# Kernel tuning notes

Hardware: AMD Instinct MI355X
Metric: run time of the kernel (lower is better)

The kernel has to match this reference:

```python
import jax, jax.numpy as jnp
import numpy as np

N1 = 50000; N2 = 50000; E1 = 800000; E2 = 800000; A = 10000
D_IN = 128; NHID = 128; D_OUT = 128; RATIO = 0.5
N_SUP = int(N1 * RATIO)  # 25000 super nodes
K_HOPS = 10  # GCN(in, nhid, k=10)
NEG_INF = jnp.float32(-1e30)


def _edge_norm(src, dst, w, n):
    # symmetric degree normalization of edge weights
    deg = jax.ops.segment_sum(w, dst, num_segments=n) + 1.0
    return w * jax.lax.rsqrt(deg[src] * deg[dst])


def _prop(h, src, dst, norm, n):
    # one round of weighted message passing: h'[v] = sum_e norm_e * h[src_e]
    return jax.ops.segment_sum(norm[:, None] * h[src], dst, num_segments=n)


def _gcn_k(x, src, dst, norm, n, W, b):
    h = x @ W + b
    for _ in range(K_HOPS):
        h = _prop(h, src, dst, norm, n)
    return h


def setup_inputs() -> dict:
    key = jax.random.key(0)
    ks = jax.random.split(key, 24)
    s = 0.05
    return {
        "x": jax.random.normal(ks[0], (N1, D_IN), jnp.float32),
        "edge_index": jax.random.randint(ks[1], (2, E1), 0, N1, jnp.int32),
        "edge_weight": jax.random.uniform(ks[2], (E1,), jnp.float32),
        "y": jax.random.normal(ks[3], (N2, D_IN), jnp.float32),
        "edge_index_y": jax.random.randint(ks[4], (2, E2), 0, N2, jnp.int32),
        "edge_weight_y": jax.random.uniform(ks[5], (E2,), jnp.float32),
        "anchor_links": jax.random.randint(ks[6], (2, A), 0, N1, jnp.int32),
        "temperature": 1,
        "W_gcn": jax.random.normal(ks[7], (D_IN, NHID), jnp.float32) * s,
        "b_gcn": jnp.zeros((NHID,), jnp.float32),
        "p_score": jax.random.normal(ks[8], (NHID,), jnp.float32) * s,
        "W_conv1": jax.random.normal(ks[9], (NHID, NHID), jnp.float32) * s,
        "b_conv1": jnp.zeros((NHID,), jnp.float32),
        "W_mlp1": jax.random.normal(ks[10], (NHID, NHID), jnp.float32) * s,
        "b_mlp1": jnp.zeros((NHID,), jnp.float32),
        "W_l1": jax.random.normal(ks[11], (NHID, NHID), jnp.float32) * s,
        "W_l2": jax.random.normal(ks[12], (NHID, NHID), jnp.float32) * s,
        "W_mlp2": jax.random.normal(ks[13], (NHID, D_OUT), jnp.float32) * s,
        "b_mlp2": jnp.zeros((D_OUT,), jnp.float32),
    }


def reference(x, edge_index, edge_weight, y, edge_index_y, edge_weight_y,
              anchor_links, temperature, W_gcn, b_gcn, p_score, W_conv1,
              b_conv1, W_mlp1, b_mlp1, W_l1, W_l2, W_mlp2, b_mlp2):
    T = jnp.float32(temperature)
    src, dst = edge_index[0], edge_index[1]
    norm1 = _edge_norm(src, dst, edge_weight, N1)

    # ---- down_convs[0]: 10-hop GCN on graph 1 ----
    out_x = _gcn_k(x, src, dst, norm1, N1, W_gcn, b_gcn)  # xs[0]
    xr = jax.nn.relu(out_x)

    # ---- TransPool: score -> top-k super nodes -> attention assignment ----
    s = xr @ p_score                             # [N1]
    _, perm = jax.lax.top_k(s, N_SUP)            # original ids of super nodes
    sup_id = jnp.full((N1,), -1, jnp.int32).at[perm].set(
        jnp.arange(N_SUP, dtype=jnp.int32))
    self_ids = jnp.arange(N1, dtype=src.dtype)
    cand_node = jnp.concatenate([src, self_ids])  # node being assigned
    cand_sup = jnp.concatenate([dst, self_ids])   # candidate super node
    valid = sup_id[cand_sup] >= 0
    att = jnp.sum(xr[cand_node] * xr[cand_sup], axis=-1)
    att = att / (jnp.sqrt(jnp.float32(NHID)) * T)
    att = jnp.where(valid, att, NEG_INF)
    m = jax.ops.segment_max(att, cand_node, num_segments=N1)
    e = jnp.exp(att - m[cand_node])
    esum = jax.ops.segment_sum(e, cand_node, num_segments=N1)
    w_soft = e / esum[cand_node]                 # per-node softmax over candidates
    is_best = valid & (att >= m[cand_node])
    cluster = jnp.full((N1,), -1, jnp.int32).at[cand_node].max(
        jnp.where(is_best, sup_id[cand_sup], -1))
    has = cluster >= 0
    cluster = jnp.maximum(cluster, 0)
    match = is_best & (sup_id[cand_sup] == cluster[cand_node])
    a = jnp.zeros((N1,), jnp.float32).at[cand_node].max(
        jnp.where(match, w_soft, 0.0))
    a = jnp.where(has, a, 0.0)                   # assign_weight (P1 values)

    # coarsen: x' = P x ; A' = P A P^T via cluster relabeling
    x_pool = jax.ops.segment_sum(a[:, None] * xr, cluster, num_segments=N_SUP)
    csrc, cdst = cluster[src], cluster[dst]
    cw = edge_weight * a[src] * a[dst]

    # ---- down_convs[1]: GCNConv on coarse graph (with self loop) ----
    norm_c = _edge_norm(csrc, cdst, cw, N_SUP)
    h2 = x_pool @ W_conv1 + b_conv1
    h2 = _prop(h2, csrc, cdst, norm_c, N_SUP) + h2
    sup1 = jax.nn.relu(h2)                       # xs[1]

    # ---- MLP1 ----
    sup2 = jax.nn.relu(sup1 @ W_mlp1 + b_mlp1)

    # ---- Q = P1 @ L (sparse-sparse matmul) ----
    a1, a2 = anchor_links[0], anchor_links[1]
    anchor_w = jnp.ones((A,), jnp.float32)
    q_sup = cluster[a1]
    q_col = a2
    q_w = a[a1] * anchor_w

    # ---- graph 2: shared down_convs[0] ----
    srcy, dsty = edge_index_y[0], edge_index_y[1]
    normy = _edge_norm(srcy, dsty, edge_weight_y, N2)
    out_y = _gcn_k(y, srcy, dsty, normy, N2, W_gcn, b_gcn)

    # ---- LastLayer: Q^T (sup2 W_l1) + L^T (out_x W_l2) scattered into graph2 ----
    t1 = sup2 @ W_l1
    out_y = out_y + jax.ops.segment_sum(q_w[:, None] * t1[q_sup], q_col,
                                        num_segments=N2)
    t2 = out_x @ W_l2
    out_y = out_y + jax.ops.segment_sum(anchor_w[:, None] * t2[a1], a2,
                                        num_segments=N2)

    recon_y = out_y @ W_mlp2 + b_mlp2
    return (out_x, sup1, out_y, sup2, a, recon_y)
```

## Files before the change

kernel.cpp:

```cpp
#include <hip/hip_runtime.h>
#include <hip/hip_bf16.h>
#include <math.h>

#define N1 50000
#define N2 50000
#define E1C 800000
#define E2C 800000
#define AC 10000
#define F 128
#define NSUP 25000
#define KHOPS 10
#define NEGINF -1e30f
#define NBINS 65536
#define NBINS22 (1 << 22)

static inline int cdiv(int a, int b) { return (a + b - 1) / b; }

__device__ __forceinline__ float bf2f(unsigned short u) {
  return __uint_as_float(((unsigned)u) << 16);
}
__device__ __forceinline__ unsigned short f2bf(float f) {
  unsigned x = __float_as_uint(f);
  return (unsigned short)((x + 0x7FFFu + ((x >> 16) & 1u)) >> 16);
}

__global__ void k_count(const int* __restrict__ key, int* __restrict__ cnt, int n) {
  int e = blockIdx.x * blockDim.x + threadIdx.x;
  if (e < n) atomicAdd(&cnt[key[e]], 1);
}

__global__ void k_scan(const int* __restrict__ cnt, int* __restrict__ rowptr, int n) {
  const int T = 1024;
  int t = threadIdx.x;
  int vpt = (n + T - 1) / T;
  int lo = t * vpt, hi = lo + vpt;
  if (hi > n) hi = n;
  int sum = 0;
  for (int i = lo; i < hi; ++i) sum += cnt[i];
  int lane = t & 63, wid = t >> 6;
  int v = sum;
#pragma unroll
  for (int o = 1; o < 64; o <<= 1) {
    int u = __shfl_up(v, o, 64);
    if (lane >= o) v += u;
  }
  __shared__ int wsum[16];
  if (lane == 63) wsum[wid] = v;
  __syncthreads();
  if (t < 16) {
    int w = wsum[t];
#pragma unroll
    for (int o = 1; o < 16; o <<= 1) {
      int u = __shfl_up(w, o, 64);
      if (t >= o) w += u;
    }
    wsum[t] = w;
  }
  __syncthreads();
  int base = (wid ? wsum[wid - 1] : 0) + (v - sum);
  if (t == 0) rowptr[0] = 0;
  int run = base;
  for (int i = lo; i < hi; ++i) { run += cnt[i]; rowptr[i + 1] = run; }
}

__global__ void k_fill(const int* __restrict__ key, const int* __restrict__ payload,
                       const float* __restrict__ val, const int* __restrict__ rowptr,
                       int* __restrict__ cnt, int* __restrict__ col, float* __restrict__ v,
                       int n) {
  int e = blockIdx.x * blockDim.x + threadIdx.x;
  if (e < n) {
    int k = key[e];
    int p = atomicAdd(&cnt[k], 1);
    int s = rowptr[k] + p;
    col[s] = payload[e];
    if (val) v[s] = val[e];
  }
}

__global__ void k_fill_iota(const int* __restrict__ key, const int* __restrict__ rowptr,
                            int* __restrict__ cnt, int* __restrict__ col, int n) {
  int e = blockIdx.x * blockDim.x + threadIdx.x;
  if (e < n) {
    int k = key[e];
    int p = atomicAdd(&cnt[k], 1);
    col[rowptr[k] + p] = e;
  }
}

__global__ void k_count_coarse(const int* __restrict__ dst, const int* __restrict__ cluster,
                               int* __restrict__ cnt, int n) {
  int e = blockIdx.x * blockDim.x + threadIdx.x;
  if (e < n) atomicAdd(&cnt[cluster[dst[e]]], 1);
}

__global__ void k_fill_coarse(const int* __restrict__ src, const int* __restrict__ dst,
                              const int* __restrict__ cluster, const float* __restrict__ w,
                              const float* __restrict__ a, const int* __restrict__ rowptr,
                              int* __restrict__ cnt, int* __restrict__ col,
                              float* __restrict__ v, int n) {
  int e = blockIdx.x * blockDim.x + threadIdx.x;
  if (e < n) {
    int sd = dst[e];
    int k = cluster[sd];
    int p = atomicAdd(&cnt[k], 1);
    int s = rowptr[k] + p;
    int ss = src[e];
    col[s] = cluster[ss];
    v[s] = w[e] * a[ss] * a[sd];
  }
}

__global__ void k_rowsum(const int* __restrict__ rowptr, const float* __restrict__ v,
                         float* __restrict__ deg, int n) {
  int row = blockIdx.x * 8 + (threadIdx.x >> 5);
  if (row >= n) return;
  int q = threadIdx.x & 31;
  int s0 = rowptr[row], s1 = rowptr[row + 1];
  float s = 0.f;
  for (int k = s0 + q; k < s1; k += 32) s += v[k];
#pragma unroll
  for (int o = 16; o; o >>= 1) s += __shfl_xor(s, o, 64);
  if (q == 0) deg[row] = s;
}

__global__ void k_csrnorm(const int* __restrict__ rowptr, const int* __restrict__ col,
                          float* __restrict__ v, const float* __restrict__ deg, int n) {
  int row = blockIdx.x * 8 + (threadIdx.x >> 5);
  if (row >= n) return;
  int q = threadIdx.x & 31;
  int s0 = rowptr[row], s1 = rowptr[row + 1];
  float di = deg[row] + 1.f;
  for (int s = s0 + q; s < s1; s += 32) {
    float dc = deg[col[s]] + 1.f;
    v[s] = v[s] / sqrtf(dc * di);
  }
}

__global__ void k_prop(const float4* __restrict__ hin, float4* __restrict__ hout,
                       float4* __restrict__ relu_out, const int* __restrict__ rowptr,
                       const int* __restrict__ col, const float* __restrict__ val, int n) {
  int node = blockIdx.x * 8 + (threadIdx.x >> 5);
  if (node >= n) return;
  int q = threadIdx.x & 31;
  int grp = threadIdx.x & 32;
  int s0 = rowptr[node], s1 = rowptr[node + 1];
  float4 acc = make_float4(0.f, 0.f, 0.f, 0.f);
  for (int s = s0; s < s1; s += 32) {
    int es = s + q;
    int ok = es < s1;
    int sc = ok ? es : (s1 - 1);
    int cme = col[sc];
    float vme = ok ? val[sc] : 0.f;
    int nb = s1 - s; if (nb > 32) nb = 32;
    for (int j = 0; j < nb; j += 8) {
      int c8[8]; float v8[8];
#pragma unroll
      for (int t = 0; t < 8; ++t) {
        c8[t] = __shfl(cme, grp + j + t, 64);
        v8[t] = __shfl(vme, grp + j + t, 64);
      }
      float4 h[8];
#pragma unroll
      for (int t = 0; t < 8; ++t) h[t] = hin[(size_t)c8[t] * 32 + q];
#pragma unroll
      for (int t = 0; t < 8; ++t) {
        acc.x = fmaf(v8[t], h[t].x, acc.x);
        acc.y = fmaf(v8[t], h[t].y, acc.y);
        acc.z = fmaf(v8[t], h[t].z, acc.z);
        acc.w = fmaf(v8[t], h[t].w, acc.w);
      }
    }
  }
  hout[(size_t)node * 32 + q] = acc;
  if (relu_out) {
    float4 r;
    r.x = fmaxf(acc.x, 0.f); r.y = fmaxf(acc.y, 0.f);
    r.z = fmaxf(acc.z, 0.f); r.w = fmaxf(acc.w, 0.f);
    relu_out[(size_t)node * 32 + q] = r;
  }
}

__global__ void k_prop_dual(const float4* __restrict__ hin1, float4* __restrict__ hout1,
                            float4* __restrict__ xr_out,
                            const int* __restrict__ rp1, const int* __restrict__ col1,
                            const float* __restrict__ val1,
                            const ushort4* __restrict__ hin2, ushort4* __restrict__ hout2,
                            float4* __restrict__ fout2,
                            const int* __restrict__ rp2, const int* __restrict__ col2,
                            const float* __restrict__ val2, int n) {
  int node = (blockIdx.x >> 1) * 8 + (threadIdx.x >> 5);
  if (node >= n) return;
  int q = threadIdx.x & 31;
  int grp = threadIdx.x & 32;
  if ((blockIdx.x & 1) == 0) {
    int s0 = rp1[node], s1 = rp1[node + 1];
    float4 acc = make_float4(0.f, 0.f, 0.f, 0.f);
    for (int s = s0; s < s1; s += 32) {
      int es = s + q;
      int ok = es < s1;
      int sc = ok ? es : (s1 - 1);
      int cme = col1[sc];
      float vme = ok ? val1[sc] : 0.f;
      int nb = s1 - s; if (nb > 32) nb = 32;
      for (int j = 0; j < nb; j += 8) {
        int c8[8]; float v8[8];
#pragma unroll
        for (int t = 0; t < 8; ++t) {
          c8[t] = __shfl(cme, grp + j + t, 64);
          v8[t] = __shfl(vme, grp + j + t, 64);
        }
        float4 h[8];
#pragma unroll
        for (int t = 0; t < 8; ++t) h[t] = hin1[(size_t)c8[t] * 32 + q];
#pragma unroll
        for (int t = 0; t < 8; ++t) {
          acc.x = fmaf(v8[t], h[t].x, acc.x);
          acc.y = fmaf(v8[t], h[t].y, acc.y);
          acc.z = fmaf(v8[t], h[t].z, acc.z);
          acc.w = fmaf(v8[t], h[t].w, acc.w);
        }
      }
    }
    hout1[(size_t)node * 32 + q] = acc;
    if (xr_out) {
      float4 r;
      r.x = fmaxf(acc.x, 0.f); r.y = fmaxf(acc.y, 0.f);
      r.z = fmaxf(acc.z, 0.f); r.w = fmaxf(acc.w, 0.f);
      xr_out[(size_t)node * 32 + q] = r;
    }
  } else {
    int s0 = rp2[node], s1 = rp2[node + 1];
    float4 acc = make_float4(0.f, 0.f, 0.f, 0.f);
    for (int s = s0; s < s1; s += 32) {
      int es = s + q;
      int ok = es < s1;
      int sc = ok ? es : (s1 - 1);
      int cme = col2[sc];
      float vme = ok ? val2[sc] : 0.f;
      int nb = s1 - s; if (nb > 32) nb = 32;
      for (int j = 0; j < nb; j += 8) {
        int c8[8]; float v8[8];
#pragma unroll
        for (int t = 0; t < 8; ++t) {
          c8[t] = __shfl(cme, grp + j + t, 64);
          v8[t] = __shfl(vme, grp + j + t, 64);
        }
        ushort4 h[8];
#pragma unroll
        for (int t = 0; t < 8; ++t) h[t] = hin2[(size_t)c8[t] * 32 + q];
#pragma unroll
        for (int t = 0; t < 8; ++t) {
          acc.x = fmaf(v8[t], bf2f(h[t].x), acc.x);
          acc.y = fmaf(v8[t], bf2f(h[t].y), acc.y);
          acc.z = fmaf(v8[t], bf2f(h[t].z), acc.z);
          acc.w = fmaf(v8[t], bf2f(h[t].w), acc.w);
        }
      }
    }
    if (fout2) {
      fout2[(size_t)node * 32 + q] = acc;
    } else {
      ushort4 o;
      o.x = f2bf(acc.x); o.y = f2bf(acc.y); o.z = f2bf(acc.z); o.w = f2bf(acc.w);
      hout2[(size_t)node * 32 + q] = o;
    }
  }
}

__global__ void k_transpose(const float* __restrict__ W, float* __restrict__ WT) {
  int i = blockIdx.x * blockDim.x + threadIdx.x;
  if (i < F * F) { int k = i >> 7, c = i & 127; WT[c * F + k] = W[i]; }
}

__global__ void k_mm128(const float* __restrict__ X, const float* __restrict__ WT,
                        const float* __restrict__ bias, float* __restrict__ out,
                        int M, int relu) {
  __shared__ float4 xs[16][32];
  int tid = threadIdx.x;
  int c = tid & 127;
  int half = tid >> 7;
  int row0 = blockIdx.x * 16;
  for (int t = tid; t < 512; t += 256) {
    int r = t >> 5, k4 = t & 31;
    int gr = row0 + r;
    float4 v = make_float4(0.f, 0.f, 0.f, 0.f);
    if (gr < M) v = ((const float4*)X)[(size_t)gr * 32 + k4];
    xs[r][k4] = v;
  }
  __syncthreads();
  float acc[8];
#pragma unroll
  for (int r = 0; r < 8; ++r) acc[r] = 0.f;
  const float4* wrow = (const float4*)WT + (size_t)c * 32;
  for (int k4 = 0; k4 < 32; ++k4) {
    float4 w = wrow[k4];
#pragma unroll
    for (int r = 0; r < 8; ++r) {
      float4 xv = xs[half * 8 + r][k4];
      acc[r] = fmaf(xv.x, w.x, acc[r]);
      acc[r] = fmaf(xv.y, w.y, acc[r]);
      acc[r] = fmaf(xv.z, w.z, acc[r]);
      acc[r] = fmaf(xv.w, w.w, acc[r]);
    }
  }
  float bb = bias ? bias[c] : 0.f;
#pragma unroll
  for (int r = 0; r < 8; ++r) {
    int gr = row0 + half * 8 + r;
    if (gr < M) {
      float v = acc[r] + bb;
      if (relu) v = fmaxf(v, 0.f);
      out[(size_t)gr * F + c] = v;
    }
  }
}

__global__ void k_mm128_bf16(const float* __restrict__ X, const float* __restrict__ WT,
                             const float* __restrict__ bias, unsigned short* __restrict__ out,
                             int M) {
  __shared__ float4 xs[16][32];
  int tid = threadIdx.x;
  int c = tid & 127;
  int half = tid >> 7;
  int row0 = blockIdx.x * 16;
  for (int t = tid; t < 512; t += 256) {
    int r = t >> 5, k4 = t & 31;
    int gr = row0 + r;
    float4 v = make_float4(0.f, 0.f, 0.f, 0.f);
    if (gr < M) v = ((const float4*)X)[(size_t)gr * 32 + k4];
    xs[r][k4] = v;
  }
  __syncthreads();
  float acc[8];
#pragma unroll
  for (int r = 0; r < 8; ++r) acc[r] = 0.f;
  const float4* wrow = (const float4*)WT + (size_t)c * 32;
  for (int k4 = 0; k4 < 32; ++k4) {
    float4 w = wrow[k4];
#pragma unroll
    for (int r = 0; r < 8; ++r) {
      float4 xv = xs[half * 8 + r][k4];
      acc[r] = fmaf(xv.x, w.x, acc[r]);
      acc[r] = fmaf(xv.y, w.y, acc[r]);
      acc[r] = fmaf(xv.z, w.z, acc[r]);
      acc[r] = fmaf(xv.w, w.w, acc[r]);
    }
  }
  float bb = bias ? bias[c] : 0.f;
#pragma unroll
  for (int r = 0; r < 8; ++r) {
    int gr = row0 + half * 8 + r;
    if (gr < M) out[(size_t)gr * F + c] = f2bf(acc[r] + bb);
  }
}

__global__ void k_addrelu(const float* __restrict__ a, const float* __restrict__ b,
                          float* __restrict__ out, int n) {
  int i = blockIdx.x * blockDim.x + threadIdx.x;
  if (i < n) out[i] = fmaxf(a[i] + b[i], 0.f);
}

__global__ void k_score(const float* __restrict__ xr, const float* __restrict__ p,
                        float* __restrict__ s, int n) {
  int wid = (blockIdx.x * blockDim.x + threadIdx.x) >> 6;
  int lane = threadIdx.x & 63;
  if (wid >= n) return;
  const float* row = xr + (size_t)wid * F;
  float d = row[lane] * p[lane] + row[lane + 64] * p[lane + 64];
#pragma unroll
  for (int o = 32; o; o >>= 1) d += __shfl_xor(d, o, 64);
  if (lane == 0) s[wid] = d;
}

__device__ __forceinline__ unsigned sortkey(float f) {
  if (f == 0.f) f = 0.f;
  unsigned u = __float_as_uint(f);
  return (u & 0x80000000u) ? ~u : (u | 0x80000000u);
}

__global__ void k_key(const float* __restrict__ s, unsigned* __restrict__ key, int n) {
  int i = blockIdx.x * blockDim.x + threadIdx.x;
  if (i < n) key[i] = sortkey(s[i]);
}

__global__ void k_count_bins22(const unsigned* __restrict__ key, int* __restrict__ cnt, int n) {
  int i = blockIdx.x * blockDim.x + threadIdx.x;
  if (i < n) atomicAdd(&cnt[key[i] >> 10], 1);
}

__global__ void k_hist_blocksum(const int* __restrict__ cnt, int* __restrict__ partial) {
  int t = threadIdx.x;
  int base = blockIdx.x * 1024 + t * 4;
  int s = cnt[base] + cnt[base + 1] + cnt[base + 2] + cnt[base + 3];
#pragma unroll
  for (int o = 32; o; o >>= 1) s += __shfl_down(s, o, 64);
  __shared__ int ws[4];
  int lane = t & 63, w = t >> 6;
  if (lane == 0) ws[w] = s;
  __syncthreads();
  if (t == 0) partial[blockIdx.x] = ws[0] + ws[1] + ws[2] + ws[3];
}

__global__ void k_hist_apply(const int* __restrict__ cnt, const int* __restrict__ partialptr,
                             int* __restrict__ binptr) {
  int t = threadIdx.x;
  int base = blockIdx.x * 1024 + t * 4;
  int c0 = cnt[base], c1 = cnt[base + 1], c2 = cnt[base + 2], c3 = cnt[base + 3];
  int s = c0 + c1 + c2 + c3;
  int lane = t & 63, w = t >> 6;
  int v = s;
#pragma unroll
  for (int o = 1; o < 64; o <<= 1) {
    int u = __shfl_up(v, o, 64);
    if (lane >= o) v += u;
  }
  __shared__ int ws[4];
  if (lane == 63) ws[w] = v;
  __syncthreads();
  int wb = 0;
  for (int i = 0; i < w; ++i) wb += ws[i];
  int run = partialptr[blockIdx.x] + wb + (v - s);
  binptr[base + 1] = run + c0;
  binptr[base + 2] = run + c0 + c1;
  binptr[base + 3] = run + c0 + c1 + c2;
  binptr[base + 4] = run + s;
  if (blockIdx.x == 0 && t == 0) binptr[0] = 0;
}

__global__ void k_fill_bins22(const unsigned* __restrict__ key, const int* __restrict__ binptr,
                              int* __restrict__ cnt, int* __restrict__ bidx,
                              unsigned* __restrict__ bkey, int n) {
  int i = blockIdx.x * blockDim.x + threadIdx.x;
  if (i < n) {
    unsigned k = key[i];
    int b = k >> 10;
    int p = atomicAdd(&cnt[b], 1);
    int s = binptr[b] + p;
    bidx[s] = i;
    bkey[s] = k;
  }
}

__global__ void k_rank22(const unsigned* __restrict__ key, const int* __restrict__ binptr,
                         const int* __restrict__ bidx, const unsigned* __restrict__ bkey,
                         int* __restrict__ supid, int n) {
  int i = blockIdx.x * blockDim.x + threadIdx.x;
  if (i >= n) return;
  unsigned ki = key[i];
  int b = ki >> 10;
  int cnt = n - binptr[b + 1];
  int s1 = binptr[b + 1];
  for (int s = binptr[b]; s < s1; ++s) {
    unsigned kj = bkey[s];
    cnt += (kj > ki) || (kj == ki && bidx[s] < i);
  }
  supid[i] = (cnt < NSUP) ? cnt : -1;
}

__device__ __forceinline__ float read_T(const void* p) {
  int ib = *(const int*)p;
  float fb = __int_as_float(ib);
  if (ib >= 1 && ib < (1 << 20)) return (float)ib;
  if (fb > 1e-6f && fb < 1e6f) return fb;
  return 1.0f;
}

__global__ void k_att_a(const float* __restrict__ xr, const int* __restrict__ rowptr,
                        const int* __restrict__ col, const int* __restrict__ supid,
                        const void* __restrict__ tptr, float* __restrict__ att,
                        float* __restrict__ attself, float* __restrict__ mout, int n) {
  int wid = (blockIdx.x * blockDim.x + threadIdx.x) >> 6;
  int lane = threadIdx.x & 63;
  if (wid >= n) return;
  float inv = 1.0f / (sqrtf(128.0f) * read_T(tptr));
  const float* xn = xr + (size_t)wid * F;
  float x0 = xn[lane], x1 = xn[lane + 64];
  float d = x0 * x0 + x1 * x1;
#pragma unroll
  for (int o = 32; o; o >>= 1) d += __shfl_xor(d, o, 64);
  float av = (supid[wid] >= 0) ? d * inv : NEGINF;
  float m = av;
  if (lane == 0) attself[wid] = av;
  int s0 = rowptr[wid], s1 = rowptr[wid + 1];
  for (int s = s0; s < s1; s += 4) {
    int c[4]; bool ok[4];
#pragma unroll
    for (int j = 0; j < 4; ++j) {
      int ss = s + j;
      ok[j] = ss < s1;
      c[j] = col[ok[j] ? ss : (s1 - 1)];
    }
    float dd[4];
#pragma unroll
    for (int j = 0; j < 4; ++j) {
      const float* xc = xr + (size_t)c[j] * F;
      dd[j] = x0 * xc[lane] + x1 * xc[lane + 64];
    }
#pragma unroll
    for (int j = 0; j < 4; ++j) {
#pragma unroll
      for (int o = 32; o; o >>= 1) dd[j] += __shfl_xor(dd[j], o, 64);
    }
#pragma unroll
    for (int j = 0; j < 4; ++j) {
      if (ok[j]) {
        float a2 = (supid[c[j]] >= 0) ? dd[j] * inv : NEGINF;
        if (lane == 0) att[s + j] = a2;
        m = fmaxf(m, a2);
      }
    }
  }
  if (lane == 0) mout[wid] = m;
}

__global__ void k_att_b(const int* __restrict__ rowptr, const int* __restrict__ col,
                        const int* __restrict__ supid, const float* __restrict__ att,
                        const float* __restrict__ attself, const float* __restrict__ mv,
                        int* __restrict__ cluster, float* __restrict__ aout, int n) {
  int i = blockIdx.x * 8 + (threadIdx.x >> 5);
  if (i >= n) return;
  int q = threadIdx.x & 31;
  float m = mv[i];
  float as = attself[i];
  float esum = 0.f;
  int best = -1;
  if (q == 0) {
    esum = expf(as - m);
    if (as >= m) best = supid[i];
  }
  int s0 = rowptr[i], s1 = rowptr[i + 1];
  for (int s = s0 + q; s < s1; s += 32) {
    float av = att[s];
    esum += expf(av - m);
    if (av >= m) {
      int sid = supid[col[s]];
      if (sid > best) best = sid;
    }
  }
#pragma unroll
  for (int o = 16; o; o >>= 1) {
    esum += __shfl_xor(esum, o, 64);
    int ob = __shfl_xor(best, o, 64);
    if (ob > best) best = ob;
  }
  if (q == 0) {
    int has = best >= 0;
    cluster[i] = has ? best : 0;
    aout[i] = has ? 1.0f / esum : 0.0f;
  }
}

__global__ void k_xpool_pull(const float4* __restrict__ xr, const float* __restrict__ a,
                             const int* __restrict__ rowptrM, const int* __restrict__ memb,
                             float4* __restrict__ xpool, int n) {
  int c = blockIdx.x * 8 + (threadIdx.x >> 5);
  if (c >= n) return;
  int q = threadIdx.x & 31;
  int s0 = rowptrM[c], s1 = rowptrM[c + 1];
  float4 acc = make_float4(0.f, 0.f, 0.f, 0.f);
  for (int s = s0; s < s1; ++s) {
    int m = memb[s];
    float av = a[m];
    float4 h = xr[(size_t)m * 32 + q];
    acc.x = fmaf(av, h.x, acc.x);
    acc.y = fmaf(av, h.y, acc.y);
    acc.z = fmaf(av, h.z, acc.z);
    acc.w = fmaf(av, h.w, acc.w);
  }
  xpool[(size_t)c * 32 + q] = acc;
}

__global__ void k_scatter_q(const int* __restrict__ a1, const int* __restrict__ a2,
                            const int* __restrict__ cluster, const float* __restrict__ aarr,
                            const float* __restrict__ t1, float* __restrict__ outy, int nA) {
  int idx = blockIdx.x * blockDim.x + threadIdx.x;
  if (idx >= nA * F) return;
  int k = idx >> 7, f = idx & 127;
  int n1 = a1[k];
  float qw = aarr[n1];
  if (qw != 0.f)
    atomicAdd(&outy[(size_t)a2[k] * F + f], qw * t1[(size_t)cluster[n1] * F + f]);
}

__global__ void k_scatter_t2(const int* __restrict__ a1, const int* __restrict__ a2,
                             const float* __restrict__ t2, float* __restrict__ outy, int nA) {
  int idx = blockIdx.x * blockDim.x + threadIdx.x;
  if (idx >= nA * F) return;
  int k = idx >> 7, f = idx & 127;
  atomicAdd(&outy[(size_t)a2[k] * F + f], t2[(size_t)a1[k] * F + f]);
}

extern "C" void kernel_launch(void* const* d_in, const int* in_sizes, int n_in,
                              void* d_out, int out_size, void* d_ws, size_t ws_size,
                              hipStream_t stream) {
  (void)in_sizes; (void)n_in; (void)out_size; (void)ws_size;
  const float* x   = (const float*)d_in[0];
  const int*   ei  = (const int*)d_in[1];
  const float* w1  = (const float*)d_in[2];
  const float* y   = (const float*)d_in[3];
  const int*   eiy = (const int*)d_in[4];
  const float* wy  = (const float*)d_in[5];
  const int*   anc = (const int*)d_in[6];
  const void*  tmp = d_in[7];
  const float* W_gcn = (const float*)d_in[8];
  const float* b_gcn = (const float*)d_in[9];
  const float* p_sc  = (const float*)d_in[10];
  const float* W_c1  = (const float*)d_in[11];
  const float* b_c1  = (const float*)d_in[12];
  const float* W_m1  = (const float*)d_in[13];
  const float* b_m1  = (const float*)d_in[14];
  const float* W_l1  = (const float*)d_in[15];
  const float* W_l2  = (const float*)d_in[16];
  const float* W_m2  = (const float*)d_in[17];
  const float* b_m2  = (const float*)d_in[18];

  float* out   = (float*)d_out;
  float* out_x = out;
  float* sup1  = out_x + (size_t)N1 * F;
  float* out_y = sup1 + (size_t)NSUP * F;
  float* sup2  = out_y + (size_t)N2 * F;
  float* a_out = sup2 + (size_t)NSUP * F;
  float* recon = a_out + N1;

  char* wsb = (char*)d_ws;
  size_t off = 0;
  auto alloc = [&](size_t bytes) -> void* {
    void* p = wsb + off;
    off = (off + bytes + 255) & ~(size_t)255;
    return p;
  };
  float*    f_csr1v   = (float*)alloc((size_t)E1C * 4);
  int*      i_csr1c   = (int*)alloc((size_t)E1C * 4);
  int*      i_rowptr1 = (int*)alloc((size_t)(N1 + 1) * 4);
  int*      i_rowptr2 = (int*)alloc((size_t)(N2 + 1) * 4);
  float*    f_deg     = (float*)alloc((size_t)N1 * 4);
  int*      i_cnt     = (int*)alloc((size_t)(NBINS + 1) * 4);
  float*    f_ha      = (float*)alloc((size_t)N1 * F * 4);
  float*    f_hb      = (float*)alloc((size_t)N1 * F * 4);
  float*    f_xr      = (float*)alloc((size_t)N1 * F * 4);
  float*    f_s       = (float*)alloc((size_t)N1 * 4);
  unsigned* u_key     = (unsigned*)alloc((size_t)N1 * 4);
  int*      i_partial = (int*)alloc((size_t)4096 * 4);
  int*      i_partptr = (int*)alloc((size_t)4097 * 4);
  int*      i_bidx    = (int*)alloc((size_t)N1 * 4);
  unsigned* u_bkey    = (unsigned*)alloc((size_t)N1 * 4);
  int*      i_supid   = (int*)alloc((size_t)N1 * 4);
  int*      i_rowptrS = (int*)alloc((size_t)(N1 + 1) * 4);
  int*      i_csrSc   = (int*)alloc((size_t)E1C * 4);
  float*    f_att     = (float*)alloc((size_t)E1C * 4);
  float*    f_attself = (float*)alloc((size_t)N1 * 4);
  float*    f_m       = (float*)alloc((size_t)N1 * 4);
  int*      i_cluster = (int*)alloc((size_t)N1 * 4);
  float*    f_xpool   = (float*)alloc((size_t)NSUP * F * 4);
  float*    f_degc    = (float*)alloc((size_t)NSUP * 4);
  int*      i_rowptrC = (int*)alloc((size_t)(NSUP + 1) * 4);
  int*      i_csrCc   = (int*)alloc((size_t)E1C * 4);
  float*    f_csrCv   = (float*)alloc((size_t)E1C * 4);
  int*      i_rowptrM = (int*)alloc((size_t)(NSUP + 1) * 4);
  int*      i_memb    = (int*)alloc((size_t)N1 * 4);
  float*    f_h2      = (float*)alloc((size_t)NSUP * F * 4);
  float*    f_h2p     = (float*)alloc((size_t)NSUP * F * 4);
  float*    f_wt      = (float*)alloc((size_t)6 * F * F * 4);

  int* i_cnt22    = (int*)f_ha;
  int* i_binptr22 = (int*)f_hb;
  int*   i_csr2c  = i_csrCc;
  float* f_csr2v  = f_csrCv;
  unsigned short* h16a = (unsigned short*)f_xpool;
  unsigned short* h16b = (unsigned short*)f_h2;

  const int* src1 = ei,  * dst1 = ei + E1C;
  const int* srcy = eiy, * dsty = eiy + E2C;
  const int* a1 = anc, * a2 = anc + AC;

  const float* Ws[6] = { W_gcn, W_c1, W_m1, W_l1, W_l2, W_m2 };
  for (int i = 0; i < 6; ++i)
    k_transpose<<<cdiv(F * F, 256), 256, 0, stream>>>(Ws[i], f_wt + (size_t)i * F * F);
  float* wt_gcn = f_wt, *wt_c1 = f_wt + 16384, *wt_m1 = f_wt + 2 * 16384,
       * wt_l1 = f_wt + 3 * 16384, *wt_l2 = f_wt + 4 * 16384, *wt_m2 = f_wt + 5 * 16384;

  int gE = cdiv(E1C, 256);
  int gN = cdiv(N1, 256);
  int gN8 = cdiv(N1, 8);
  int gC8 = cdiv(NSUP, 8);
  int gD = 2 * cdiv(N1, 8);

  hipMemsetAsync(i_cnt, 0, (size_t)(NBINS + 1) * 4, stream);
  k_count<<<gE, 256, 0, stream>>>(dst1, i_cnt, E1C);
  k_scan<<<1, 1024, 0, stream>>>(i_cnt, i_rowptr1, N1);
  hipMemsetAsync(i_cnt, 0, (size_t)(NBINS + 1) * 4, stream);
  k_fill<<<gE, 256, 0, stream>>>(dst1, src1, w1, i_rowptr1, i_cnt, i_csr1c, f_csr1v, E1C);
  k_rowsum<<<gN8, 256, 0, stream>>>(i_rowptr1, f_csr1v, f_deg, N1);
  k_csrnorm<<<gN8, 256, 0, stream>>>(i_rowptr1, i_csr1c, f_csr1v, f_deg, N1);

  hipMemsetAsync(i_cnt, 0, (size_t)(NBINS + 1) * 4, stream);
  k_count<<<gE, 256, 0, stream>>>(dsty, i_cnt, E2C);
  k_scan<<<1, 1024, 0, stream>>>(i_cnt, i_rowptr2, N2);
  hipMemsetAsync(i_cnt, 0, (size_t)(NBINS + 1) * 4, stream);
  k_fill<<<gE, 256, 0, stream>>>(dsty, srcy, wy, i_rowptr2, i_cnt, i_csr2c, f_csr2v, E2C);
  k_rowsum<<<gN8, 256, 0, stream>>>(i_rowptr2, f_csr2v, f_deg, N2);
  k_csrnorm<<<gN8, 256, 0, stream>>>(i_rowptr2, i_csr2c, f_csr2v, f_deg, N2);

  k_mm128<<<cdiv(N1, 16), 256, 0, stream>>>(x, wt_gcn, b_gcn, f_ha, N1, 0);
  k_mm128_bf16<<<cdiv(N2, 16), 256, 0, stream>>>(y, wt_gcn, b_gcn, h16a, N2);

  {
    const float* cur1 = f_ha;
    const unsigned short* cur2 = h16a;
    for (int i = 0; i < KHOPS; ++i) {
      int last = (i == KHOPS - 1);
      float* dst1b = last ? out_x : ((i & 1) ? f_ha : f_hb);
      unsigned short* dst2b = (i & 1) ? h16a : h16b;
      k_prop_dual<<<gD, 256, 0, stream>>>(
          (const float4*)cur1, (float4*)dst1b, last ? (float4*)f_xr : nullptr,
          i_rowptr1, i_csr1c, f_csr1v,
          (const ushort4*)cur2, (ushort4*)dst2b, last ? (float4*)out_y : nullptr,
          i_rowptr2, i_csr2c, f_csr2v, N1);
      cur1 = dst1b; cur2 = dst2b;
    }
  }

  k_score<<<cdiv(N1, 4), 256, 0, stream>>>(f_xr, p_sc, f_s, N1);
  k_key<<<gN, 256, 0, stream>>>(f_s, u_key, N1);
  hipMemsetAsync(i_cnt22, 0, (size_t)NBINS22 * 4, stream);
  k_count_bins22<<<gN, 256, 0, stream>>>(u_key, i_cnt22, N1);
  k_hist_blocksum<<<NBINS22 / 1024, 256, 0, stream>>>(i_cnt22, i_partial);
  k_scan<<<1, 1024, 0, stream>>>(i_partial, i_partptr, 4096);
  k_hist_apply<<<NBINS22 / 1024, 256, 0, stream>>>(i_cnt22, i_partptr, i_binptr22);
  hipMemsetAsync(i_cnt22, 0, (size_t)NBINS22 * 4, stream);
  k_fill_bins22<<<gN, 256, 0, stream>>>(u_key, i_binptr22, i_cnt22, i_bidx, u_bkey, N1);
  k_rank22<<<gN, 256, 0, stream>>>(u_key, i_binptr22, i_bidx, u_bkey, i_supid, N1);

  hipMemsetAsync(i_cnt, 0, (size_t)(NBINS + 1) * 4, stream);
  k_count<<<gE, 256, 0, stream>>>(src1, i_cnt, E1C);
  k_scan<<<1, 1024, 0, stream>>>(i_cnt, i_rowptrS, N1);
  hipMemsetAsync(i_cnt, 0, (size_t)(NBINS + 1) * 4, stream);
  k_fill<<<gE, 256, 0, stream>>>(src1, dst1, (const float*)nullptr, i_rowptrS, i_cnt, i_csrSc,
                                 (float*)nullptr, E1C);

  k_att_a<<<cdiv(N1, 4), 256, 0, stream>>>(f_xr, i_rowptrS, i_csrSc, i_supid, tmp,
                                           f_att, f_attself, f_m, N1);
  k_att_b<<<gN8, 256, 0, stream>>>(i_rowptrS, i_csrSc, i_supid, f_att, f_attself,
                                   f_m, i_cluster, a_out, N1);

  hipMemsetAsync(i_cnt, 0, (size_t)(NBINS + 1) * 4, stream);
  k_count<<<gN, 256, 0, stream>>>(i_cluster, i_cnt, N1);
  k_scan<<<1, 1024, 0, stream>>>(i_cnt, i_rowptrM, NSUP);
  hipMemsetAsync(i_cnt, 0, (size_t)(NBINS + 1) * 4, stream);
  k_fill_iota<<<gN, 256, 0, stream>>>(i_cluster, i_rowptrM, i_cnt, i_memb, N1);
  k_xpool_pull<<<gC8, 256, 0, stream>>>((const float4*)f_xr, a_out, i_rowptrM,
                                        i_memb, (float4*)f_xpool, NSUP);

  hipMemsetAsync(i_cnt, 0, (size_t)(NBINS + 1) * 4, stream);
  k_count_coarse<<<gE, 256, 0, stream>>>(dst1, i_cluster, i_cnt, E1C);
  k_scan<<<1, 1024, 0, stream>>>(i_cnt, i_rowptrC, NSUP);
  hipMemsetAsync(i_cnt, 0, (size_t)(NBINS + 1) * 4, stream);
  k_fill_coarse<<<gE, 256, 0, stream>>>(src1, dst1, i_cluster, w1, a_out, i_rowptrC, i_cnt,
                                        i_csrCc, f_csrCv, E1C);
  k_rowsum<<<gC8, 256, 0, stream>>>(i_rowptrC, f_csrCv, f_degc, NSUP);
  k_csrnorm<<<gC8, 256, 0, stream>>>(i_rowptrC, i_csrCc, f_csrCv, f_degc, NSUP);

  k_mm128<<<cdiv(NSUP, 16), 256, 0, stream>>>(f_xpool, wt_c1, b_c1, f_h2, NSUP, 0);
  k_prop<<<gC8, 256, 0, stream>>>((const float4*)f_h2, (float4*)f_h2p, nullptr,
                                  i_rowptrC, i_csrCc, f_csrCv, NSUP);
  k_addrelu<<<cdiv(NSUP * F, 256), 256, 0, stream>>>(f_h2p, f_h2, sup1, NSUP * F);
  k_mm128<<<cdiv(NSUP, 16), 256, 0, stream>>>(sup1, wt_m1, b_m1, sup2, NSUP, 1);

  float* f_t1 = f_h2p;
  float* f_t2 = f_xr;
  k_mm128<<<cdiv(NSUP, 16), 256, 0, stream>>>(sup2, wt_l1, (const float*)nullptr, f_t1, NSUP, 0);
  k_scatter_q<<<cdiv(AC * F, 256), 256, 0, stream>>>(a1, a2, i_cluster, a_out, f_t1, out_y, AC);
  k_mm128<<<cdiv(N1, 16), 256, 0, stream>>>(out_x, wt_l2, (const float*)nullptr, f_t2, N1, 0);
  k_scatter_t2<<<cdiv(AC * F, 256), 256, 0, stream>>>(a1, a2, f_t2, out_y, AC);

  k_mm128<<<cdiv(N2, 16), 256, 0, stream>>>(out_y, wt_m2, b_m2, recon, N2, 0);
}
```

Before: 2.357 ms.

## Batch CSR builds, fuse attention passes, and drop counter re-zeroing memsets

Builds the three edge CSRs (graph1 by dst, graph2 by dst, graph1 by src) in one count/scan/fill pass. The fill step decrements the counters, so no re-zeroing memsets are needed between stages. The two-pass attention softmax/argmax becomes a single online-softmax kernel, removing the per-edge attention buffer. Several small kernels are also merged: six transposes into one, score plus key, the two anchor scatters, and the coarse prop with its add+relu. The aim is fewer launches and less intermediate memory traffic. The online softmax changes the order of floating-point accumulation, and the CSR slot order within a row is now reversed.

Result: faster. 2.122 ms (-10.0%).

```diff
diff --git a/kernel.cpp b/kernel.cpp
--- a/kernel.cpp
+++ b/kernel.cpp
@@ -11,7 +11,7 @@
 #define NSUP 25000
 #define KHOPS 10
 #define NEGINF -1e30f
-#define NBINS 65536
+#define NB 65536
 #define NBINS22 (1 << 22)
 
 static inline int cdiv(int a, int b) { return (a + b - 1) / b; }
@@ -29,7 +29,16 @@
   if (e < n) atomicAdd(&cnt[key[e]], 1);
 }
 
-__global__ void k_scan(const int* __restrict__ cnt, int* __restrict__ rowptr, int n) {
+__global__ void k_count3(const int* __restrict__ d1, const int* __restrict__ dy,
+                         const int* __restrict__ s1, int* __restrict__ cnt3) {
+  int e = blockIdx.x * blockDim.x + threadIdx.x;
+  if (e >= 3 * E1C) return;
+  int g = e / E1C, i = e - g * E1C;
+  int key = (g == 0) ? d1[i] : (g == 1) ? dy[i] : s1[i];
+  atomicAdd(&cnt3[g * NB + key], 1);
+}
+
+__device__ __forceinline__ void scan_body(const int* cnt, int* rowptr, int n) {
   const int T = 1024;
   int t = threadIdx.x;
   int vpt = (n + T - 1) / T;
@@ -63,17 +72,46 @@
   for (int i = lo; i < hi; ++i) { run += cnt[i]; rowptr[i + 1] = run; }
 }
 
-__global__ void k_fill(const int* __restrict__ key, const int* __restrict__ payload,
-                       const float* __restrict__ val, const int* __restrict__ rowptr,
-                       int* __restrict__ cnt, int* __restrict__ col, float* __restrict__ v,
-                       int n) {
+__global__ void k_scan(const int* __restrict__ cnt, int* __restrict__ rowptr, int n) {
+  scan_body(cnt, rowptr, n);
+}
+
+__global__ void k_scan3(const int* __restrict__ cnt3, int* __restrict__ rp0,
+                        int* __restrict__ rp1, int* __restrict__ rp2,
+                        int n0, int n1, int n2) {
+  int b = blockIdx.x;
+  const int* cnt = cnt3 + b * NB;
+  int* rowptr = (b == 0) ? rp0 : (b == 1) ? rp1 : rp2;
+  int n = (b == 0) ? n0 : (b == 1) ? n1 : n2;
+  scan_body(cnt, rowptr, n);
+}
+
+__global__ void k_fill3(const int* __restrict__ d1, const int* __restrict__ s1,
+                        const float* __restrict__ w1,
+                        const int* __restrict__ dy, const int* __restrict__ sy,
+                        const float* __restrict__ wy,
+                        const int* __restrict__ rp1, const int* __restrict__ rp2,
+                        const int* __restrict__ rpS, int* __restrict__ cnt3,
+                        int* __restrict__ c1, float* __restrict__ v1,
+                        int* __restrict__ c2, float* __restrict__ v2,
+                        int* __restrict__ cS) {
   int e = blockIdx.x * blockDim.x + threadIdx.x;
-  if (e < n) {
-    int k = key[e];
-    int p = atomicAdd(&cnt[k], 1);
-    int s = rowptr[k] + p;
-    col[s] = payload[e];
-    if (val) v[s] = val[e];
+  if (e >= 3 * E1C) return;
+  int g = e / E1C, i = e - g * E1C;
+  if (g == 0) {
+    int k = d1[i];
+    int p = atomicSub(&cnt3[k], 1) - 1;
+    int s = rp1[k] + p;
+    c1[s] = s1[i]; v1[s] = w1[i];
+  } else if (g == 1) {
+    int k = dy[i];
+    int p = atomicSub(&cnt3[NB + k], 1) - 1;
+    int s = rp2[k] + p;
+    c2[s] = sy[i]; v2[s] = wy[i];
+  } else {
+    int k = s1[i];
+    int p = atomicSub(&cnt3[2 * NB + k], 1) - 1;
+    cS[rpS[k] + p] = d1[i];
   }
 }
 
@@ -82,7 +120,7 @@
   int e = blockIdx.x * blockDim.x + threadIdx.x;
   if (e < n) {
     int k = key[e];
-    int p = atomicAdd(&cnt[k], 1);
+    int p = atomicSub(&cnt[k], 1) - 1;
     col[rowptr[k] + p] = e;
   }
 }
@@ -102,7 +140,7 @@
   if (e < n) {
     int sd = dst[e];
     int k = cluster[sd];
-    int p = atomicAdd(&cnt[k], 1);
+    int p = atomicSub(&cnt[k], 1) - 1;
     int s = rowptr[k] + p;
     int ss = src[e];
     col[s] = cluster[ss];
@@ -136,8 +174,42 @@
   }
 }
 
+__global__ void k_rowsum2(const int* __restrict__ rpA, const float* __restrict__ vA,
+                          float* __restrict__ degA, int nA,
+                          const int* __restrict__ rpB, const float* __restrict__ vB,
+                          float* __restrict__ degB, int nB) {
+  int row = blockIdx.x * 8 + (threadIdx.x >> 5);
+  const int* rp; const float* v; float* deg; int r;
+  if (row < nA) { rp = rpA; v = vA; deg = degA; r = row; }
+  else { r = row - nA; if (r >= nB) return; rp = rpB; v = vB; deg = degB; }
+  int q = threadIdx.x & 31;
+  int s0 = rp[r], s1 = rp[r + 1];
+  float s = 0.f;
+  for (int k = s0 + q; k < s1; k += 32) s += v[k];
+#pragma unroll
+  for (int o = 16; o; o >>= 1) s += __shfl_xor(s, o, 64);
+  if (q == 0) deg[r] = s;
+}
+
+__global__ void k_csrnorm2(const int* __restrict__ rpA, const int* __restrict__ colA,
+                           float* __restrict__ vA, const float* __restrict__ degA, int nA,
+                           const int* __restrict__ rpB, const int* __restrict__ colB,
+                           float* __restrict__ vB, const float* __restrict__ degB, int nB) {
+  int row = blockIdx.x * 8 + (threadIdx.x >> 5);
+  const int* rp; const int* col; float* v; const float* deg; int r;
+  if (row < nA) { rp = rpA; col = colA; v = vA; deg = degA; r = row; }
+  else { r = row - nA; if (r >= nB) return; rp = rpB; col = colB; v = vB; deg = degB; }
+  int q = threadIdx.x & 31;
+  int s0 = rp[r], s1 = rp[r + 1];
+  float di = deg[r] + 1.f;
+  for (int s = s0 + q; s < s1; s += 32) {
+    float dc = deg[col[s]] + 1.f;
+    v[s] = v[s] / sqrtf(dc * di);
+  }
+}
+
 __global__ void k_prop(const float4* __restrict__ hin, float4* __restrict__ hout,
-                       float4* __restrict__ relu_out, const int* __restrict__ rowptr,
+                       const float4* __restrict__ addin, const int* __restrict__ rowptr,
                        const int* __restrict__ col, const float* __restrict__ val, int n) {
   int node = blockIdx.x * 8 + (threadIdx.x >> 5);
   if (node >= n) return;
@@ -171,12 +243,14 @@
       }
     }
   }
-  hout[(size_t)node * 32 + q] = acc;
-  if (relu_out) {
+  if (addin) {
+    float4 ad = addin[(size_t)node * 32 + q];
     float4 r;
-    r.x = fmaxf(acc.x, 0.f); r.y = fmaxf(acc.y, 0.f);
-    r.z = fmaxf(acc.z, 0.f); r.w = fmaxf(acc.w, 0.f);
-    relu_out[(size_t)node * 32 + q] = r;
+    r.x = fmaxf(acc.x + ad.x, 0.f); r.y = fmaxf(acc.y + ad.y, 0.f);
+    r.z = fmaxf(acc.z + ad.z, 0.f); r.w = fmaxf(acc.w + ad.w, 0.f);
+    hout[(size_t)node * 32 + q] = r;
+  } else {
+    hout[(size_t)node * 32 + q] = acc;
   }
 }
 
@@ -267,9 +341,16 @@
   }
 }
 
-__global__ void k_transpose(const float* __restrict__ W, float* __restrict__ WT) {
+__global__ void k_transpose6(const float* __restrict__ W0, const float* __restrict__ W1,
+                             const float* __restrict__ W2, const float* __restrict__ W3,
+                             const float* __restrict__ W4, const float* __restrict__ W5,
+                             float* __restrict__ WT) {
   int i = blockIdx.x * blockDim.x + threadIdx.x;
-  if (i < F * F) { int k = i >> 7, c = i & 127; WT[c * F + k] = W[i]; }
+  if (i >= 6 * F * F) return;
+  int w = i >> 14, r = i & 16383, k = r >> 7, c = r & 127;
+  const float* W = (w == 0) ? W0 : (w == 1) ? W1 : (w == 2) ? W2
+                   : (w == 3) ? W3 : (w == 4) ? W4 : W5;
+  WT[(size_t)w * 16384 + c * F + k] = W[r];
 }
 
 __global__ void k_mm128(const float* __restrict__ X, const float* __restrict__ WT,
@@ -354,14 +435,14 @@
   }
 }
 
-__global__ void k_addrelu(const float* __restrict__ a, const float* __restrict__ b,
-                          float* __restrict__ out, int n) {
-  int i = blockIdx.x * blockDim.x + threadIdx.x;
-  if (i < n) out[i] = fmaxf(a[i] + b[i], 0.f);
-}
-
-__global__ void k_score(const float* __restrict__ xr, const float* __restrict__ p,
-                        float* __restrict__ s, int n) {
+__device__ __forceinline__ unsigned sortkey(float f) {
+  if (f == 0.f) f = 0.f;
+  unsigned u = __float_as_uint(f);
+  return (u & 0x80000000u) ? ~u : (u | 0x80000000u);
+}
+
+__global__ void k_score_key(const float* __restrict__ xr, const float* __restrict__ p,
+                            unsigned* __restrict__ key, int n) {
   int wid = (blockIdx.x * blockDim.x + threadIdx.x) >> 6;
   int lane = threadIdx.x & 63;
   if (wid >= n) return;
@@ -369,18 +450,7 @@
   float d = row[lane] * p[lane] + row[lane + 64] * p[lane + 64];
 #pragma unroll
   for (int o = 32; o; o >>= 1) d += __shfl_xor(d, o, 64);
-  if (lane == 0) s[wid] = d;
-}
-
-__device__ __forceinline__ unsigned sortkey(float f) {
-  if (f == 0.f) f = 0.f;
-  unsigned u = __float_as_uint(f);
-  return (u & 0x80000000u) ? ~u : (u | 0x80000000u);
-}
-
-__global__ void k_key(const float* __restrict__ s, unsigned* __restrict__ key, int n) {
-  int i = blockIdx.x * blockDim.x + threadIdx.x;
-  if (i < n) key[i] = sortkey(s[i]);
+  if (lane == 0) key[wid] = sortkey(d);
 }
 
 __global__ void k_count_bins22(const unsigned* __restrict__ key, int* __restrict__ cnt, int n) {
@@ -434,7 +504,7 @@
   if (i < n) {
     unsigned k = key[i];
     int b = k >> 10;
-    int p = atomicAdd(&cnt[b], 1);
+    int p = atomicSub(&cnt[b], 1) - 1;
     int s = binptr[b] + p;
     bidx[s] = i;
     bkey[s] = k;
@@ -465,10 +535,10 @@
   return 1.0f;
 }
 
-__global__ void k_att_a(const float* __restrict__ xr, const int* __restrict__ rowptr,
-                        const int* __restrict__ col, const int* __restrict__ supid,
-                        const void* __restrict__ tptr, float* __restrict__ att,
-                        float* __restrict__ attself, float* __restrict__ mout, int n) {
+__global__ void k_att(const float* __restrict__ xr, const int* __restrict__ rowptr,
+                      const int* __restrict__ col, const int* __restrict__ supid,
+                      const void* __restrict__ tptr,
+                      int* __restrict__ cluster, float* __restrict__ aout, int n) {
   int wid = (blockIdx.x * blockDim.x + threadIdx.x) >> 6;
   int lane = threadIdx.x & 63;
   if (wid >= n) return;
@@ -478,9 +548,10 @@
   float d = x0 * x0 + x1 * x1;
 #pragma unroll
   for (int o = 32; o; o >>= 1) d += __shfl_xor(d, o, 64);
-  float av = (supid[wid] >= 0) ? d * inv : NEGINF;
-  float m = av;
-  if (lane == 0) attself[wid] = av;
+  int sid_self = supid[wid];
+  float m = (sid_self >= 0) ? d * inv : NEGINF;
+  float esum = 1.0f;
+  int best = sid_self;
   int s0 = rowptr[wid], s1 = rowptr[wid + 1];
   for (int s = s0; s < s1; s += 4) {
     int c[4]; bool ok[4];
@@ -504,49 +575,23 @@
 #pragma unroll
     for (int j = 0; j < 4; ++j) {
       if (ok[j]) {
-        float a2 = (supid[c[j]] >= 0) ? dd[j] * inv : NEGINF;
-        if (lane == 0) att[s + j] = a2;
-        m = fmaxf(m, a2);
+        int sid = supid[c[j]];
+        float a2 = (sid >= 0) ? dd[j] * inv : NEGINF;
+        if (a2 > m) {
+          esum = esum * expf(m - a2) + 1.0f;
+          m = a2;
+          best = sid;
+        } else {
+          esum += expf(a2 - m);
+          if (a2 == m && sid > best) best = sid;
+        }
       }
     }
   }
-  if (lane == 0) mout[wid] = m;
-}
-
-__global__ void k_att_b(const int* __restrict__ rowptr, const int* __restrict__ col,
-                        const int* __restrict__ supid, const float* __restrict__ att,
-                        const float* __restrict__ attself, const float* __restrict__ mv,
-                        int* __restrict__ cluster, float* __restrict__ aout, int n) {
-  int i = blockIdx.x * 8 + (threadIdx.x >> 5);
-  if (i >= n) return;
-  int q = threadIdx.x & 31;
-  float m = mv[i];
-  float as = attself[i];
-  float esum = 0.f;
-  int best = -1;
-  if (q == 0) {
-    esum = expf(as - m);
-    if (as >= m) best = supid[i];
-  }
-  int s0 = rowptr[i], s1 = rowptr[i + 1];
-  for (int s = s0 + q; s < s1; s += 32) {
-    float av = att[s];
-    esum += expf(av - m);
-    if (av >= m) {
-      int sid = supid[col[s]];
-      if (sid > best) best = sid;
-    }
-  }
-#pragma unroll
-  for (int o = 16; o; o >>= 1) {
-    esum += __shfl_xor(esum, o, 64);
-    int ob = __shfl_xor(best, o, 64);
-    if (ob > best) best = ob;
-  }
-  if (q == 0) {
+  if (lane == 0) {
     int has = best >= 0;
-    cluster[i] = has ? best : 0;
-    aout[i] = has ? 1.0f / esum : 0.0f;
+    cluster[wid] = has ? best : 0;
+    aout[wid] = has ? 1.0f / esum : 0.0f;
   }
 }
 
@@ -570,24 +615,18 @@
   xpool[(size_t)c * 32 + q] = acc;
 }
 
-__global__ void k_scatter_q(const int* __restrict__ a1, const int* __restrict__ a2,
-                            const int* __restrict__ cluster, const float* __restrict__ aarr,
-                            const float* __restrict__ t1, float* __restrict__ outy, int nA) {
+__global__ void k_scatter2(const int* __restrict__ a1, const int* __restrict__ a2,
+                           const int* __restrict__ cluster, const float* __restrict__ aarr,
+                           const float* __restrict__ t1, const float* __restrict__ t2,
+                           float* __restrict__ outy, int nA) {
   int idx = blockIdx.x * blockDim.x + threadIdx.x;
   if (idx >= nA * F) return;
   int k = idx >> 7, f = idx & 127;
   int n1 = a1[k];
+  float add = t2[(size_t)n1 * F + f];
   float qw = aarr[n1];
-  if (qw != 0.f)
-    atomicAdd(&outy[(size_t)a2[k] * F + f], qw * t1[(size_t)cluster[n1] * F + f]);
-}
-
-__global__ void k_scatter_t2(const int* __restrict__ a1, const int* __restrict__ a2,
-                             const float* __restrict__ t2, float* __restrict__ outy, int nA) {
-  int idx = blockIdx.x * blockDim.x + threadIdx.x;
-  if (idx >= nA * F) return;
-  int k = idx >> 7, f = idx & 127;
-  atomicAdd(&outy[(size_t)a2[k] * F + f], t2[(size_t)a1[k] * F + f]);
+  if (qw != 0.f) add += qw * t1[(size_t)cluster[n1] * F + f];
+  atomicAdd(&outy[(size_t)a2[k] * F + f], add);
 }
 
 extern "C" void kernel_launch(void* const* d_in, const int* in_sizes, int n_in,
@@ -634,11 +673,11 @@
   int*      i_rowptr1 = (int*)alloc((size_t)(N1 + 1) * 4);
   int*      i_rowptr2 = (int*)alloc((size_t)(N2 + 1) * 4);
   float*    f_deg     = (float*)alloc((size_t)N1 * 4);
-  int*      i_cnt     = (int*)alloc((size_t)(NBINS + 1) * 4);
+  float*    f_deg2    = (float*)alloc((size_t)N2 * 4);
+  int*      i_cnt3    = (int*)alloc((size_t)3 * NB * 4);
   float*    f_ha      = (float*)alloc((size_t)N1 * F * 4);
   float*    f_hb      = (float*)alloc((size_t)N1 * F * 4);
   float*    f_xr      = (float*)alloc((size_t)N1 * F * 4);
-  float*    f_s       = (float*)alloc((size_t)N1 * 4);
   unsigned* u_key     = (unsigned*)alloc((size_t)N1 * 4);
   int*      i_partial = (int*)alloc((size_t)4096 * 4);
   int*      i_partptr = (int*)alloc((size_t)4097 * 4);
@@ -647,9 +686,6 @@
   int*      i_supid   = (int*)alloc((size_t)N1 * 4);
   int*      i_rowptrS = (int*)alloc((size_t)(N1 + 1) * 4);
   int*      i_csrSc   = (int*)alloc((size_t)E1C * 4);
-  float*    f_att     = (float*)alloc((size_t)E1C * 4);
-  float*    f_attself = (float*)alloc((size_t)N1 * 4);
-  float*    f_m       = (float*)alloc((size_t)N1 * 4);
   int*      i_cluster = (int*)alloc((size_t)N1 * 4);
   float*    f_xpool   = (float*)alloc((size_t)NSUP * F * 4);
   float*    f_degc    = (float*)alloc((size_t)NSUP * 4);
@@ -673,33 +709,27 @@
   const int* srcy = eiy, * dsty = eiy + E2C;
   const int* a1 = anc, * a2 = anc + AC;
 
-  const float* Ws[6] = { W_gcn, W_c1, W_m1, W_l1, W_l2, W_m2 };
-  for (int i = 0; i < 6; ++i)
-    k_transpose<<<cdiv(F * F, 256), 256, 0, stream>>>(Ws[i], f_wt + (size_t)i * F * F);
+  int gE = cdiv(E1C, 256);
+  int gN = cdiv(N1, 256);
+  int gC8 = cdiv(NSUP, 8);
+  int gD = 2 * cdiv(N1, 8);
+
+  hipMemsetAsync(i_cnt3, 0, (size_t)3 * NB * 4, stream);
+  k_transpose6<<<cdiv(6 * F * F, 256), 256, 0, stream>>>(W_gcn, W_c1, W_m1, W_l1, W_l2,
+                                                         W_m2, f_wt);
   float* wt_gcn = f_wt, *wt_c1 = f_wt + 16384, *wt_m1 = f_wt + 2 * 16384,
        * wt_l1 = f_wt + 3 * 16384, *wt_l2 = f_wt + 4 * 16384, *wt_m2 = f_wt + 5 * 16384;
 
-  int gE = cdiv(E1C, 256);
-  int gN = cdiv(N1, 256);
-  int gN8 = cdiv(N1, 8);
-  int gC8 = cdiv(NSUP, 8);
-  int gD = 2 * cdiv(N1, 8);
-
-  hipMemsetAsync(i_cnt, 0, (size_t)(NBINS + 1) * 4, stream);
-  k_count<<<gE, 256, 0, stream>>>(dst1, i_cnt, E1C);
-  k_scan<<<1, 1024, 0, stream>>>(i_cnt, i_rowptr1, N1);
-  hipMemsetAsync(i_cnt, 0, (size_t)(NBINS + 1) * 4, stream);
-  k_fill<<<gE, 256, 0, stream>>>(dst1, src1, w1, i_rowptr1, i_cnt, i_csr1c, f_csr1v, E1C);
-  k_rowsum<<<gN8, 256, 0, stream>>>(i_rowptr1, f_csr1v, f_deg, N1);
-  k_csrnorm<<<gN8, 256, 0, stream>>>(i_rowptr1, i_csr1c, f_csr1v, f_deg, N1);
-
-  hipMemsetAsync(i_cnt, 0, (size_t)(NBINS + 1) * 4, stream);
-  k_count<<<gE, 256, 0, stream>>>(dsty, i_cnt, E2C);
-  k_scan<<<1, 1024, 0, stream>>>(i_cnt, i_rowptr2, N2);
-  hipMemsetAsync(i_cnt, 0, (size_t)(NBINS + 1) * 4, stream);
-  k_fill<<<gE, 256, 0, stream>>>(dsty, srcy, wy, i_rowptr2, i_cnt, i_csr2c, f_csr2v, E2C);
-  k_rowsum<<<gN8, 256, 0, stream>>>(i_rowptr2, f_csr2v, f_deg, N2);
-  k_csrnorm<<<gN8, 256, 0, stream>>>(i_rowptr2, i_csr2c, f_csr2v, f_deg, N2);
+  k_count3<<<cdiv(3 * E1C, 256), 256, 0, stream>>>(dst1, dsty, src1, i_cnt3);
+  k_scan3<<<3, 1024, 0, stream>>>(i_cnt3, i_rowptr1, i_rowptr2, i_rowptrS, N1, N2, N1);
+  k_fill3<<<cdiv(3 * E1C, 256), 256, 0, stream>>>(dst1, src1, w1, dsty, srcy, wy,
+                                                  i_rowptr1, i_rowptr2, i_rowptrS, i_cnt3,
+                                                  i_csr1c, f_csr1v, i_csr2c, f_csr2v,
+                                                  i_csrSc);
+  k_rowsum2<<<cdiv(N1 + N2, 8), 256, 0, stream>>>(i_rowptr1, f_csr1v, f_deg, N1,
+                                                  i_rowptr2, f_csr2v, f_deg2, N2);
+  k_csrnorm2<<<cdiv(N1 + N2, 8), 256, 0, stream>>>(i_rowptr1, i_csr1c, f_csr1v, f_deg, N1,
+                                                   i_rowptr2, i_csr2c, f_csr2v, f_deg2, N2);
 
   k_mm128<<<cdiv(N1, 16), 256, 0, stream>>>(x, wt_gcn, b_gcn, f_ha, N1, 0);
   k_mm128_bf16<<<cdiv(N2, 16), 256, 0, stream>>>(y, wt_gcn, b_gcn, h16a, N2);
@@ -720,58 +750,44 @@
     }
   }
 
-  k_score<<<cdiv(N1, 4), 256, 0, stream>>>(f_xr, p_sc, f_s, N1);
-  k_key<<<gN, 256, 0, stream>>>(f_s, u_key, N1);
+  k_score_key<<<cdiv(N1, 4), 256, 0, stream>>>(f_xr, p_sc, u_key, N1);
   hipMemsetAsync(i_cnt22, 0, (size_t)NBINS22 * 4, stream);
   k_count_bins22<<<gN, 256, 0, stream>>>(u_key, i_cnt22, N1);
   k_hist_blocksum<<<NBINS22 / 1024, 256, 0, stream>>>(i_cnt22, i_partial);
   k_scan<<<1, 1024, 0, stream>>>(i_partial, i_partptr, 4096);
   k_hist_apply<<<NBINS22 / 1024, 256, 0, stream>>>(i_cnt22, i_partptr, i_binptr22);
-  hipMemsetAsync(i_cnt22, 0, (size_t)NBINS22 * 4, stream);
   k_fill_bins22<<<gN, 256, 0, stream>>>(u_key, i_binptr22, i_cnt22, i_bidx, u_bkey, N1);
   k_rank22<<<gN, 256, 0, stream>>>(u_key, i_binptr22, i_bidx, u_bkey, i_supid, N1);
 
-  hipMemsetAsync(i_cnt, 0, (size_t)(NBINS + 1) * 4, stream);
-  k_count<<<gE, 256, 0, stream>>>(src1, i_cnt, E1C);
-  k_scan<<<1, 1024, 0, stream>>>(i_cnt, i_rowptrS, N1);
-  hipMemsetAsync(i_cnt, 0, (size_t)(NBINS + 1) * 4, stream);
-  k_fill<<<gE, 256, 0, stream>>>(src1, dst1, (const float*)nullptr, i_rowptrS, i_cnt, i_csrSc,
-                                 (float*)nullptr, E1C);
-
-  k_att_a<<<cdiv(N1, 4), 256, 0, stream>>>(f_xr, i_rowptrS, i_csrSc, i_supid, tmp,
-                                           f_att, f_attself, f_m, N1);
-  k_att_b<<<gN8, 256, 0, stream>>>(i_rowptrS, i_csrSc, i_supid, f_att, f_attself,
-                                   f_m, i_cluster, a_out, N1);
-
-  hipMemsetAsync(i_cnt, 0, (size_t)(NBINS + 1) * 4, stream);
-  k_count<<<gN, 256, 0, stream>>>(i_cluster, i_cnt, N1);
-  k_scan<<<1, 1024, 0, stream>>>(i_cnt, i_rowptrM, NSUP);
-  hipMemsetAsync(i_cnt, 0, (size_t)(NBINS + 1) * 4, stream);
-  k_fill_iota<<<gN, 256, 0, stream>>>(i_cluster, i_rowptrM, i_cnt, i_memb, N1);
+  k_att<<<cdiv(N1, 4), 256, 0, stream>>>(f_xr, i_rowptrS, i_csrSc, i_supid, tmp,
+                                         i_cluster, a_out, N1);
+
+  k_count<<<gN, 256, 0, stream>>>(i_cluster, i_cnt3, N1);
+  k_scan<<<1, 1024, 0, stream>>>(i_cnt3, i_rowptrM, NSUP);
+  k_fill_iota<<<gN, 256, 0, stream>>>(i_cluster, i_rowptrM, i_cnt3, i_memb, N1);
   k_xpool_pull<<<gC8, 256, 0, stream>>>((const float4*)f_xr, a_out, i_rowptrM,
                                         i_memb, (float4*)f_xpool, NSUP);
 
-  hipMemsetAsync(i_cnt, 0, (size_t)(NBINS + 1) * 4, stream);
-  k_count_coarse<<<gE, 256, 0, stream>>>(dst1, i_cluster, i_cnt, E1C);
-  k_scan<<<1, 1024, 0, stream>>>(i_cnt, i_rowptrC, NSUP);
-  hipMemsetAsync(i_cnt, 0, (size_t)(NBINS + 1) * 4, stream);
-  k_fill_coarse<<<gE, 256, 0, stream>>>(src1, dst1, i_cluster, w1, a_out, i_rowptrC, i_cnt,
+  k_count_coarse<<<gE, 256, 0, stream>>>(dst1, i_cluster, i_cnt3, E1C);
+  k_scan<<<1, 1024, 0, stream>>>(i_cnt3, i_rowptrC, NSUP);
+  k_fill_coarse<<<gE, 256, 0, stream>>>(src1, dst1, i_cluster, w1, a_out, i_rowptrC, i_cnt3,
                                         i_csrCc, f_csrCv, E1C);
   k_rowsum<<<gC8, 256, 0, stream>>>(i_rowptrC, f_csrCv, f_degc, NSUP);
   k_csrnorm<<<gC8, 256, 0, stream>>>(i_rowptrC, i_csrCc, f_csrCv, f_degc, NSUP);
 
   k_mm128<<<cdiv(NSUP, 16), 256, 0, stream>>>(f_xpool, wt_c1, b_c1, f_h2, NSUP, 0);
-  k_prop<<<gC8, 256, 0, stream>>>((const float4*)f_h2, (float4*)f_h2p, nullptr,
+  k_prop<<<gC8, 256, 0, stream>>>((const float4*)f_h2, (float4*)sup1, (const float4*)f_h2,
                                   i_rowptrC, i_csrCc, f_csrCv, NSUP);
-  k_addrelu<<<cdiv(NSUP * F, 256), 256, 0, stream>>>(f_h2p, f_h2, sup1, NSUP * F);
   k_mm128<<<cdiv(NSUP, 16), 256, 0, stream>>>(sup1, wt_m1, b_m1, sup2, NSUP, 1);
 
   float* f_t1 = f_h2p;
   float* f_t2 = f_xr;
-  k_mm128<<<cdiv(NSUP, 16), 256, 0, stream>>>(sup2, wt_l1, (const float*)nullptr, f_t1, NSUP, 0);
-  k_scatter_q<<<cdiv(AC * F, 256), 256, 0, stream>>>(a1, a2, i_cluster, a_out, f_t1, out_y, AC);
-  k_mm128<<<cdiv(N1, 16), 256, 0, stream>>>(out_x, wt_l2, (const float*)nullptr, f_t2, N1, 0);
-  k_scatter_t2<<<cdiv(AC * F, 256), 256, 0, stream>>>(a1, a2, f_t2, out_y, AC);
+  k_mm128<<<cdiv(NSUP, 16), 256, 0, stream>>>(sup2, wt_l1, (const float*)nullptr, f_t1,
+                                              NSUP, 0);
+  k_mm128<<<cdiv(N1, 16), 256, 0, stream>>>(out_x, wt_l2, (const float*)nullptr, f_t2,
+                                            N1, 0);
+  k_scatter2<<<cdiv(AC * F, 256), 256, 0, stream>>>(a1, a2, i_cluster, a_out, f_t1, f_t2,
+                                                    out_y, AC);
 
   k_mm128<<<cdiv(N2, 16), 256, 0, stream>>>(out_y, wt_m2, b_m2, recon, N2, 0);
 }
```
